# Kernel optimization log

Measured on AMD Instinct MI355X. Metric: run time of the kernel, lower is better.

## Reference

```python
import jax, jax.numpy as jnp
import numpy as np

N = 100000      # nodes
E = 1600000     # edges (before self loops)
F_IN = 128
HID = 32
H = 4
OUT = 32
NEG_SLOPE = 0.2


def setup_inputs() -> dict:
    key = jax.random.key(0)
    ks = jax.random.split(key, 10)
    x = jax.random.normal(ks[0], (N, F_IN), jnp.float32)
    edge_index = jax.random.randint(ks[1], (2, E), 0, N, jnp.int32)
    s1 = 1.0 / np.sqrt(F_IN)
    s2 = 1.0 / np.sqrt(H * HID)
    W1 = jax.random.normal(ks[2], (F_IN, H * HID), jnp.float32) * s1
    a_src1 = jax.random.normal(ks[3], (H, HID), jnp.float32) * 0.1
    a_dst1 = jax.random.normal(ks[4], (H, HID), jnp.float32) * 0.1
    b1 = jnp.zeros((H * HID,), jnp.float32)
    W2 = jax.random.normal(ks[5], (H * HID, OUT), jnp.float32) * s2
    a_src2 = jax.random.normal(ks[6], (1, OUT), jnp.float32) * 0.1
    a_dst2 = jax.random.normal(ks[7], (1, OUT), jnp.float32) * 0.1
    b2 = jnp.zeros((OUT,), jnp.float32)
    return {"x": x, "edge_index": edge_index, "W1": W1, "a_src1": a_src1,
            "a_dst1": a_dst1, "b1": b1, "W2": W2, "a_src2": a_src2,
            "a_dst2": a_dst2, "b2": b2}


def gat_conv(x, src, dst, W, a_src, a_dst, b, heads, out_ch):
    # PyG GATConv (concat=True) with self loops already appended to src/dst.
    n = x.shape[0]
    h = (x @ W).reshape(n, heads, out_ch)                 # [N,H,C]
    alpha_s = jnp.sum(h * a_src, axis=-1)                 # [N,H]
    alpha_d = jnp.sum(h * a_dst, axis=-1)                 # [N,H]
    e = jax.nn.leaky_relu(alpha_s[src] + alpha_d[dst], NEG_SLOPE)  # [E',H]
    # segment softmax over destination nodes (self loops => every segment nonempty)
    emax = jax.ops.segment_max(e, dst, num_segments=n)
    ex = jnp.exp(e - emax[dst])
    denom = jax.ops.segment_sum(ex, dst, num_segments=n)
    alpha = ex / denom[dst]                               # [E',H]
    msg = h[src] * alpha[:, :, None]                      # [E',H,C]
    out = jax.ops.segment_sum(msg, dst, num_segments=n)   # [N,H,C]
    return out.reshape(n, heads * out_ch) + b


def reference(x, edge_index, W1, a_src1, a_dst1, b1, W2, a_src2, a_dst2, b2):
    loops = jnp.arange(N, dtype=edge_index.dtype)
    src = jnp.concatenate([edge_index[0], loops])
    dst = jnp.concatenate([edge_index[1], loops])
    h = gat_conv(x, src, dst, W1, a_src1, a_dst1, b1, H, HID)
    h = jax.nn.relu(h)                                    # dropout: eval mode, no-op
    out = gat_conv(h, src, dst, W2, a_src2, a_dst2, b2, 1, OUT)
    return out
```

## Files before the change

kernel.cpp:

```cpp
#include <hip/hip_runtime.h>
#include <hip/hip_fp16.h>

#define NEG 0.2f
#define EPB 4096
#define BSH 6
#define SLOT 48
#define KBMAX 1664

typedef _Float16 half8 __attribute__((ext_vector_type(8)));
typedef float f32x4 __attribute__((ext_vector_type(4)));

__global__ void k_prep(const float* __restrict__ W1, const float* __restrict__ W2,
                       half8* __restrict__ Wp, half8* __restrict__ W2p,
                       int* __restrict__ gcount, int KB) {
    int b = blockIdx.x;
    if (b < 8) {
        int u = b * 256 + threadIdx.x;
        int s = u >> 9, tn = (u >> 6) & 7, lane = u & 63;
        int quad = lane >> 4, c = lane & 15;
        half8 v;
#pragma unroll
        for (int j = 0; j < 8; ++j)
            v[j] = (_Float16)W1[(s * 32 + quad * 8 + j) * 128 + tn * 16 + c];
        Wp[u] = v;
    } else if (b < 10) {
        int u = (b - 8) * 256 + threadIdx.x;
        int n = u >> 8, s = (u >> 6) & 3, lane = u & 63;
        int quad = lane >> 4, c = lane & 15;
        half8 v;
#pragma unroll
        for (int j = 0; j < 8; ++j)
            v[j] = (_Float16)W2[(s * 32 + quad * 8 + j) * 32 + n * 16 + c];
        W2p[u] = v;
    } else {
        int i = (b - 10) * 256 + threadIdx.x;
        if (i < KB) gcount[i] = 0;
    }
}

__global__ __launch_bounds__(256) void k_pA(const float* __restrict__ x,
                                            const half8* __restrict__ Wp,
                                            const float* __restrict__ a_s,
                                            const float* __restrict__ a_d,
                                            __half* __restrict__ h1h,
                                            float* __restrict__ as1,
                                            float* __restrict__ ad1, int N,
                                            const int* __restrict__ dstp,
                                            int* __restrict__ gcount,
                                            int* __restrict__ blkoff,
                                            int E, int KB, int ngemm) {
    __shared__ _Float16 xa[64][136];
    __shared__ int lh[KBMAX];
    int t = threadIdx.x;

    if (blockIdx.x >= ngemm) {
        int blk = blockIdx.x - ngemm;
        for (int i = t; i < KB; i += 256) lh[i] = 0;
        __syncthreads();
        int base0 = blk * EPB;
#pragma unroll 4
        for (int j = 0; j < EPB / 256; ++j) {
            int i = base0 + j * 256 + t;
            if (i < E) atomicAdd(&lh[dstp[i] >> BSH], 1);
        }
        __syncthreads();
        for (int b = t; b < KB; b += 256) {
            int c = lh[b];
            if (c > 0) blkoff[(size_t)blk * KB + b] = atomicAdd(&gcount[b], c);
        }
        return;
    }

    int row0 = blockIdx.x * 64;
    {
        int row = t >> 2;
        int col0 = (t & 3) * 32;
        int gr = row0 + row;
        const float4* xsrc = (const float4*)&x[(size_t)gr * 128 + col0];
#pragma unroll
        for (int m = 0; m < 4; ++m) {
            float4 p0, p1;
            if (gr < N) { p0 = xsrc[m * 2]; p1 = xsrc[m * 2 + 1]; }
            else { p0 = float4{0,0,0,0}; p1 = float4{0,0,0,0}; }
            _Float16* dstq = &xa[row][col0 + m * 8];
            dstq[0] = (_Float16)p0.x; dstq[1] = (_Float16)p0.y;
            dstq[2] = (_Float16)p0.z; dstq[3] = (_Float16)p0.w;
            dstq[4] = (_Float16)p1.x; dstq[5] = (_Float16)p1.y;
            dstq[6] = (_Float16)p1.z; dstq[7] = (_Float16)p1.w;
        }
    }
    __syncthreads();

    int w = t >> 6;
    int lane = t & 63;
    int quad = lane >> 4, c = lane & 15;

    f32x4 acc[8];
#pragma unroll
    for (int i = 0; i < 8; ++i) acc[i] = f32x4{0, 0, 0, 0};

#pragma unroll
    for (int s = 0; s < 4; ++s) {
        half8 a = *(const half8*)&xa[w * 16 + c][s * 32 + quad * 8];
#pragma unroll
        for (int tn = 0; tn < 8; ++tn) {
            half8 b = Wp[(s * 8 + tn) * 64 + lane];
            acc[tn] = __builtin_amdgcn_mfma_f32_16x16x32_f16(a, b, acc[tn], 0, 0, 0);
        }
    }

    float asv[8], adv[8];
#pragma unroll
    for (int tn = 0; tn < 8; ++tn) { asv[tn] = a_s[tn * 16 + c]; adv[tn] = a_d[tn * 16 + c]; }
#pragma unroll
    for (int r = 0; r < 4; ++r) {
        int gr = row0 + w * 16 + quad * 4 + r;
#pragma unroll
        for (int h = 0; h < 4; ++h) {
            float ps = acc[2*h][r] * asv[2*h] + acc[2*h+1][r] * asv[2*h+1];
            float pd = acc[2*h][r] * adv[2*h] + acc[2*h+1][r] * adv[2*h+1];
            ps += __shfl_xor(ps, 1); ps += __shfl_xor(ps, 2);
            ps += __shfl_xor(ps, 4); ps += __shfl_xor(ps, 8);
            pd += __shfl_xor(pd, 1); pd += __shfl_xor(pd, 2);
            pd += __shfl_xor(pd, 4); pd += __shfl_xor(pd, 8);
            if (c == 0 && gr < N) { as1[gr * 4 + h] = ps; ad1[gr * 4 + h] = pd; }
        }
    }

    __syncthreads();
#pragma unroll
    for (int tn = 0; tn < 8; ++tn)
#pragma unroll
        for (int r = 0; r < 4; ++r)
            xa[w * 16 + quad * 4 + r][tn * 16 + c] = (_Float16)acc[tn][r];
    __syncthreads();
    {
        int row = t >> 2;
        int seg = t & 3;
        int gr = row0 + row;
        if (gr < N) {
            float4* gp = (float4*)&h1h[(size_t)gr * 128 + seg * 32];
#pragma unroll
            for (int i = 0; i < 4; ++i)
                gp[i] = *(float4*)&xa[row][seg * 32 + i * 8];
        }
    }
}

__global__ __launch_bounds__(1024) void k_scan(const int* __restrict__ gcount,
                                               int* __restrict__ gbase, int KB, int E) {
    __shared__ int s[1024];
    int t = threadIdx.x;
    int i0 = 2 * t, i1 = 2 * t + 1;
    int a = (i0 < KB) ? gcount[i0] : 0;
    int b = (i1 < KB) ? gcount[i1] : 0;
    int v = a + b;
    s[t] = v;
    __syncthreads();
    for (int off = 1; off < 1024; off <<= 1) {
        int u = (t >= off) ? s[t - off] : 0;
        __syncthreads();
        s[t] += u;
        __syncthreads();
    }
    int excl = s[t] - v;
    if (i0 < KB) gbase[i0] = excl;
    if (i1 < KB) gbase[i1] = excl + a;
    if (t == 0) gbase[KB] = E;
}

__global__ __launch_bounds__(256) void k_pB(const int* __restrict__ srcp,
                                            const int* __restrict__ dstp,
                                            const int* __restrict__ gbase,
                                            const int* __restrict__ blkoff,
                                            int2* __restrict__ ebuf, int E, int KB) {
    __shared__ int lh[KBMAX];
    int t = threadIdx.x;
    int blk = blockIdx.x;
    for (int i = t; i < KB; i += 256) lh[i] = 0;
    __syncthreads();
    int base0 = blk * EPB;
    const int* bo = &blkoff[(size_t)blk * KB];
    for (int j = 0; j < EPB / 256; j += 4) {
        int idx[4], dd[4], ss[4];
        bool ok[4];
#pragma unroll
        for (int u = 0; u < 4; ++u) {
            idx[u] = base0 + (j + u) * 256 + t;
            ok[u] = idx[u] < E;
        }
#pragma unroll
        for (int u = 0; u < 4; ++u) if (ok[u]) { dd[u] = dstp[idx[u]]; ss[u] = srcp[idx[u]]; }
#pragma unroll
        for (int u = 0; u < 4; ++u) {
            if (ok[u]) {
                int b = dd[u] >> BSH;
                int r = atomicAdd(&lh[b], 1);
                int pos = gbase[b] + bo[b] + r;
                ebuf[pos] = int2{ss[u], dd[u]};
            }
        }
    }
}

__global__ __launch_bounds__(256) void k_aggC(const int2* __restrict__ ebuf,
                                              const int* __restrict__ gbase,
                                              const __half* __restrict__ h1h,
                                              const float* __restrict__ as1,
                                              const float* __restrict__ ad1,
                                              const float* __restrict__ b1,
                                              const half8* __restrict__ W2p,
                                              const float* __restrict__ asw,
                                              const float* __restrict__ adw,
                                              int* __restrict__ csr,
                                              int* __restrict__ counts,
                                              __half* __restrict__ h2h,
                                              float* __restrict__ as2,
                                              float* __restrict__ ad2, int N) {
    __shared__ int lcnt[64];
    __shared__ int lcsr[64 * SLOT];
    __shared__ _Float16 stg[4][16][136];
    int t = threadIdx.x;
    int b = blockIdx.x, d0 = b << BSH;

    if (t < 64) lcnt[t] = 0;
    __syncthreads();

    int e0 = gbase[b], e1 = gbase[b + 1];
    for (int i = e0 + t; i < e1; i += 256) {
        int2 e = ebuf[i];
        int li = e.y - d0;
        int r = atomicAdd(&lcnt[li], 1);
        lcsr[li * SLOT + r] = e.x;
    }
    __syncthreads();

    {
        int4* gc = (int4*)&csr[(size_t)d0 * SLOT];
        const int4* lc = (const int4*)lcsr;
#pragma unroll
        for (int u = 0; u < 3; ++u) gc[t + 256 * u] = lc[t + 256 * u];
        if (t < 64 && d0 + t < N) counts[d0 + t] = lcnt[t];
    }

    int w = t >> 6, lane = t & 63;
    int quad = lane >> 4, c16 = lane & 15;
    int head = lane >> 4;
    const __half2* hp = (const __half2*)h1h;
    float2 bv = *(const float2*)&b1[2 * lane];

    half8 bf[2][4];
#pragma unroll
    for (int n = 0; n < 2; ++n)
#pragma unroll
        for (int s = 0; s < 4; ++s) bf[n][s] = W2p[(n * 4 + s) * 64 + lane];
    float asw0 = asw[c16], asw1 = asw[16 + c16];
    float adw0 = adw[c16], adw1 = adw[16 + c16];

    for (int i = 0; i < 16; ++i) {
        int dst = d0 + w * 16 + i;
        bool valid = dst < N;
        int li = w * 16 + i;
        int cnt = valid ? lcnt[li] : 0;
        int cbase = li * SLOT;
        float adv = valid ? ad1[dst * 4 + head] : 0.f;
        float ax = 0.f, ay = 0.f, den = 0.f;
        if (valid) {
            float es = as1[dst * 4 + head] + adv;
            es = es > 0.f ? es : NEG * es;
            float xs = __expf(es);
            float2 fs = __half22float2(hp[(size_t)dst * 64 + lane]);
            ax = xs * fs.x; ay = xs * fs.y; den = xs;
        }
        int e = 0;
        for (; e + 8 <= cnt; e += 8) {
            int si[8];
#pragma unroll
            for (int j = 0; j < 8; ++j) si[j] = lcsr[cbase + e + j];
            float ej[8];
#pragma unroll
            for (int j = 0; j < 8; ++j) ej[j] = as1[si[j] * 4 + head];
            __half2 vj[8];
#pragma unroll
            for (int j = 0; j < 8; ++j) vj[j] = hp[(size_t)si[j] * 64 + lane];
#pragma unroll
            for (int j = 0; j < 8; ++j) {
                float ee = ej[j] + adv;
                ee = ee > 0.f ? ee : NEG * ee;
                float xw = __expf(ee);
                float2 f = __half22float2(vj[j]);
                ax += xw * f.x; ay += xw * f.y; den += xw;
            }
        }
        for (; e + 4 <= cnt; e += 4) {
            int si[4];
#pragma unroll
            for (int j = 0; j < 4; ++j) si[j] = lcsr[cbase + e + j];
            float ej[4];
#pragma unroll
            for (int j = 0; j < 4; ++j) ej[j] = as1[si[j] * 4 + head];
            __half2 vj[4];
#pragma unroll
            for (int j = 0; j < 4; ++j) vj[j] = hp[(size_t)si[j] * 64 + lane];
#pragma unroll
            for (int j = 0; j < 4; ++j) {
                float ee = ej[j] + adv;
                ee = ee > 0.f ? ee : NEG * ee;
                float xw = __expf(ee);
                float2 f = __half22float2(vj[j]);
                ax += xw * f.x; ay += xw * f.y; den += xw;
            }
        }
        for (; e < cnt; ++e) {
            int s0 = lcsr[cbase + e];
            float e0v = as1[s0 * 4 + head] + adv;
            __half2 v0 = hp[(size_t)s0 * 64 + lane];
            e0v = e0v > 0.f ? e0v : NEG * e0v;  float x0 = __expf(e0v);
            float2 f0 = __half22float2(v0);
            ax += x0 * f0.x; ay += x0 * f0.y; den += x0;
        }
        float inv = valid ? 1.f / den : 0.f;
        float o0 = ax * inv + bv.x;
        float o1 = ay * inv + bv.y;
        o0 = o0 > 0.f ? o0 : 0.f;
        o1 = o1 > 0.f ? o1 : 0.f;
        ((__half2*)&stg[w][i][0])[lane] = __floats2half2_rn(o0, o1);
    }

    f32x4 am0 = {0, 0, 0, 0}, am1 = {0, 0, 0, 0};
#pragma unroll
    for (int s = 0; s < 4; ++s) {
        half8 a = *(const half8*)&stg[w][c16][s * 32 + quad * 8];
        am0 = __builtin_amdgcn_mfma_f32_16x16x32_f16(a, bf[0][s], am0, 0, 0, 0);
        am1 = __builtin_amdgcn_mfma_f32_16x16x32_f16(a, bf[1][s], am1, 0, 0, 0);
    }
#pragma unroll
    for (int r = 0; r < 4; ++r) {
        int dst = d0 + w * 16 + quad * 4 + r;
        float ps = am0[r] * asw0 + am1[r] * asw1;
        float pd = am0[r] * adw0 + am1[r] * adw1;
        ps += __shfl_xor(ps, 1); ps += __shfl_xor(ps, 2);
        ps += __shfl_xor(ps, 4); ps += __shfl_xor(ps, 8);
        pd += __shfl_xor(pd, 1); pd += __shfl_xor(pd, 2);
        pd += __shfl_xor(pd, 4); pd += __shfl_xor(pd, 8);
        if (dst < N) {
            h2h[(size_t)dst * 32 + c16]      = __float2half_rn(am0[r]);
            h2h[(size_t)dst * 32 + 16 + c16] = __float2half_rn(am1[r]);
            if (c16 == 0) { as2[dst] = ps; ad2[dst] = pd; }
        }
    }
}

__global__ __launch_bounds__(256) void k_agg2(const __half* __restrict__ h2h,
                                              const float* __restrict__ as2,
                                              const float* __restrict__ ad2,
                                              const int* __restrict__ csr,
                                              const int* __restrict__ counts,
                                              const float* __restrict__ b2,
                                              float* __restrict__ out, int N) {
    int w = threadIdx.x >> 6;
    int lane = threadIdx.x & 63;
    int dst = blockIdx.x * 4 + w;
    if (dst >= N) return;
    int q = lane >> 5;
    int c = lane & 31;
    float adv = ad2[dst];
    int beg = dst * SLOT;
    int cnt = counts[dst];
    float acc = 0.f, den = 0.f;
    if (q == 0) {
        float es = as2[dst] + adv;
        es = es > 0.f ? es : NEG * es;
        float xs = __expf(es);
        acc = xs * __half2float(h2h[(size_t)dst * 32 + c]);
        den = xs;
    }
    int e = q;
    for (; e + 6 < cnt; e += 8) {
        int si[4];
#pragma unroll
        for (int j = 0; j < 4; ++j) si[j] = csr[beg + e + 2 * j];
        float ej[4];
#pragma unroll
        for (int j = 0; j < 4; ++j) ej[j] = as2[si[j]];
        float vj[4];
#pragma unroll
        for (int j = 0; j < 4; ++j) vj[j] = __half2float(h2h[(size_t)si[j] * 32 + c]);
#pragma unroll
        for (int j = 0; j < 4; ++j) {
            float ee = ej[j] + adv;
            ee = ee > 0.f ? ee : NEG * ee;
            float xw = __expf(ee);
            acc += xw * vj[j];
            den += xw;
        }
    }
    for (; e < cnt; e += 2) {
        int s0 = csr[beg + e];
        float e0 = as2[s0] + adv;
        float v0 = __half2float(h2h[(size_t)s0 * 32 + c]);
        e0 = e0 > 0.f ? e0 : NEG * e0;  float x0 = __expf(e0);
        acc += x0 * v0;
        den += x0;
    }
    acc += __shfl_xor(acc, 32, 64);
    den += __shfl_xor(den, 32, 64);
    if (q == 0) out[(size_t)dst * 32 + c] = acc / den + b2[c];
}

extern "C" void kernel_launch(void* const* d_in, const int* in_sizes, int n_in,
                              void* d_out, int out_size, void* d_ws, size_t ws_size,
                              hipStream_t stream) {
    const float* x     = (const float*)d_in[0];
    const int*   ei    = (const int*)d_in[1];
    const float* W1    = (const float*)d_in[2];
    const float* as_w1 = (const float*)d_in[3];
    const float* ad_w1 = (const float*)d_in[4];
    const float* b1    = (const float*)d_in[5];
    const float* W2    = (const float*)d_in[6];
    const float* as_w2 = (const float*)d_in[7];
    const float* ad_w2 = (const float*)d_in[8];
    const float* b2    = (const float*)d_in[9];
    float* out = (float*)d_out;

    int N  = in_sizes[0] / 128;
    int E  = in_sizes[1] / 2;
    const int* srcp = ei;
    const int* dstp = ei + E;

    int KB     = (N + 63) >> BSH;
    int ND     = KB << BSH;
    int nblkB  = (E + EPB - 1) / EPB;
    int ngemm  = (N + 63) / 64;

    char* p = (char*)d_ws;
    auto alloc = [&](size_t bytes) -> char* {
        char* r = p;
        p += (bytes + 255) & ~(size_t)255;
        return r;
    };
    __half* h1h    = (__half*)alloc((size_t)N * 128 * 2);
    float*  as1    = (float*)alloc((size_t)N * 4 * 4);
    float*  ad1    = (float*)alloc((size_t)N * 4 * 4);
    __half* h2h    = (__half*)alloc((size_t)N * 32 * 2);
    float*  as2    = (float*)alloc((size_t)N * 4);
    float*  ad2    = (float*)alloc((size_t)N * 4);
    int*    counts = (int*)alloc((size_t)ND * 4);
    int*    csr    = (int*)alloc((size_t)ND * SLOT * 4);
    half8*  Wp     = (half8*)alloc(2048 * 16);
    half8*  W2p    = (half8*)alloc(512 * 16);
    int*    gcount = (int*)alloc((size_t)KB * 4);
    int*    gbase  = (int*)alloc((size_t)(KB + 1) * 4);
    int*    blkoff = (int*)alloc((size_t)nblkB * KB * 4);
    int2*   ebuf   = (int2*)alloc((size_t)E * 8);

    k_prep<<<10 + (KB + 255) / 256, 256, 0, stream>>>(W1, W2, Wp, W2p, gcount, KB);
    k_pA<<<ngemm + nblkB, 256, 0, stream>>>(x, Wp, as_w1, ad_w1, h1h, as1, ad1, N,
                                            dstp, gcount, blkoff, E, KB, ngemm);
    k_scan<<<1, 1024, 0, stream>>>(gcount, gbase, KB, E);
    k_pB<<<nblkB, 256, 0, stream>>>(srcp, dstp, gbase, blkoff, ebuf, E, KB);
    k_aggC<<<KB, 256, 0, stream>>>(ebuf, gbase, h1h, as1, ad1, b1,
                                   W2p, as_w2, ad_w2, csr, counts, h2h, as2, ad2, N);
    k_agg2<<<(N + 3) / 4, 256, 0, stream>>>(h2h, as2, ad2, csr, counts, b2, out, N);
}
```

Baseline: 318.8 us.

## Replace atomic bucket offsets with per-block histograms and column scan kernel

Result: slower. 354.8 us (+11.3%).

```diff
diff --git a/kernel.cpp b/kernel.cpp
--- a/kernel.cpp
+++ b/kernel.cpp
@@ -2,7 +2,7 @@
 #include <hip/hip_fp16.h>
 
 #define NEG 0.2f
-#define EPB 4096
+#define EPB 16384
 #define BSH 6
 #define SLOT 48
 #define KBMAX 1664
@@ -11,8 +11,7 @@
 typedef float f32x4 __attribute__((ext_vector_type(4)));
 
 __global__ void k_prep(const float* __restrict__ W1, const float* __restrict__ W2,
-                       half8* __restrict__ Wp, half8* __restrict__ W2p,
-                       int* __restrict__ gcount, int KB) {
+                       half8* __restrict__ Wp, half8* __restrict__ W2p) {
     int b = blockIdx.x;
     if (b < 8) {
         int u = b * 256 + threadIdx.x;
@@ -23,7 +22,7 @@
         for (int j = 0; j < 8; ++j)
             v[j] = (_Float16)W1[(s * 32 + quad * 8 + j) * 128 + tn * 16 + c];
         Wp[u] = v;
-    } else if (b < 10) {
+    } else {
         int u = (b - 8) * 256 + threadIdx.x;
         int n = u >> 8, s = (u >> 6) & 3, lane = u & 63;
         int quad = lane >> 4, c = lane & 15;
@@ -32,9 +31,6 @@
         for (int j = 0; j < 8; ++j)
             v[j] = (_Float16)W2[(s * 32 + quad * 8 + j) * 32 + n * 16 + c];
         W2p[u] = v;
-    } else {
-        int i = (b - 10) * 256 + threadIdx.x;
-        if (i < KB) gcount[i] = 0;
     }
 }
 
@@ -46,8 +42,7 @@
                                             float* __restrict__ as1,
                                             float* __restrict__ ad1, int N,
                                             const int* __restrict__ dstp,
-                                            int* __restrict__ gcount,
-                                            int* __restrict__ blkoff,
+                                            int* __restrict__ blkhist,
                                             int E, int KB, int ngemm) {
     __shared__ _Float16 xa[64][136];
     __shared__ int lh[KBMAX];
@@ -58,16 +53,13 @@
         for (int i = t; i < KB; i += 256) lh[i] = 0;
         __syncthreads();
         int base0 = blk * EPB;
-#pragma unroll 4
         for (int j = 0; j < EPB / 256; ++j) {
             int i = base0 + j * 256 + t;
             if (i < E) atomicAdd(&lh[dstp[i] >> BSH], 1);
         }
         __syncthreads();
-        for (int b = t; b < KB; b += 256) {
-            int c = lh[b];
-            if (c > 0) blkoff[(size_t)blk * KB + b] = atomicAdd(&gcount[b], c);
-        }
+        for (int b = t; b < KB; b += 256)
+            blkhist[(size_t)blk * KB + b] = lh[b];
         return;
     }
 
@@ -145,6 +137,21 @@
                 gp[i] = *(float4*)&xa[row][seg * 32 + i * 8];
         }
     }
+}
+
+__global__ __launch_bounds__(256) void k_colscan(int* __restrict__ bh,
+                                                 int* __restrict__ gcount,
+                                                 int KB, int nblk) {
+    int b = blockIdx.x * 256 + threadIdx.x;
+    if (b >= KB) return;
+    int run = 0;
+#pragma unroll 4
+    for (int blk = 0; blk < nblk; ++blk) {
+        int v = bh[(size_t)blk * KB + b];
+        bh[(size_t)blk * KB + b] = run;
+        run += v;
+    }
+    gcount[b] = run;
 }
 
 __global__ __launch_bounds__(1024) void k_scan(const int* __restrict__ gcount,
@@ -376,6 +383,25 @@
         den = xs;
     }
     int e = q;
+    for (; e + 14 < cnt; e += 16) {
+        int si[8];
+#pragma unroll
+        for (int j = 0; j < 8; ++j) si[j] = csr[beg + e + 2 * j];
+        float ej[8];
+#pragma unroll
+        for (int j = 0; j < 8; ++j) ej[j] = as2[si[j]];
+        float vj[8];
+#pragma unroll
+        for (int j = 0; j < 8; ++j) vj[j] = __half2float(h2h[(size_t)si[j] * 32 + c]);
+#pragma unroll
+        for (int j = 0; j < 8; ++j) {
+            float ee = ej[j] + adv;
+            ee = ee > 0.f ? ee : NEG * ee;
+            float xw = __expf(ee);
+            acc += xw * vj[j];
+            den += xw;
+        }
+    }
     for (; e + 6 < cnt; e += 8) {
         int si[4];
 #pragma unroll
@@ -451,14 +477,15 @@
     half8*  W2p    = (half8*)alloc(512 * 16);
     int*    gcount = (int*)alloc((size_t)KB * 4);
     int*    gbase  = (int*)alloc((size_t)(KB + 1) * 4);
-    int*    blkoff = (int*)alloc((size_t)nblkB * KB * 4);
+    int*    blkhist= (int*)alloc((size_t)nblkB * KB * 4);
     int2*   ebuf   = (int2*)alloc((size_t)E * 8);
 
-    k_prep<<<10 + (KB + 255) / 256, 256, 0, stream>>>(W1, W2, Wp, W2p, gcount, KB);
+    k_prep<<<10, 256, 0, stream>>>(W1, W2, Wp, W2p);
     k_pA<<<ngemm + nblkB, 256, 0, stream>>>(x, Wp, as_w1, ad_w1, h1h, as1, ad1, N,
-                                            dstp, gcount, blkoff, E, KB, ngemm);
+                                            dstp, blkhist, E, KB, ngemm);
+    k_colscan<<<(KB + 255) / 256, 256, 0, stream>>>(blkhist, gcount, KB, nblkB);
     k_scan<<<1, 1024, 0, stream>>>(gcount, gbase, KB, E);
-    k_pB<<<nblkB, 256, 0, stream>>>(srcp, dstp, gbase, blkoff, ebuf, E, KB);
+    k_pB<<<nblkB, 256, 0, stream>>>(srcp, dstp, gbase, blkhist, ebuf, E, KB);
     k_aggC<<<KB, 256, 0, stream>>>(ebuf, gbase, h1h, as1, ad1, b1,
                                    W2p, as_w2, ad_w2, csr, counts, h2h, as2, ad2, N);
     k_agg2<<<(N + 3) / 4, 256, 0, stream>>>(h2h, as2, ad2, csr, counts, b2, out, N);
```
